# Kernel tuning notes

Measured on AMD Instinct MI355X. Metric: run time of the kernel, lower is better.

## Reference

```python
import jax, jax.numpy as jnp
import numpy as np

L, B, S, D, H, DH, V = 6, 2048, 64, 256, 8, 64, 100
INNER = H * DH          # 512
FF = 4 * D              # 1024 (GeGLU hidden after chunk)
SCALE = 8.0             # sqrt(DH)


def setup_inputs() -> dict:
    key = jax.random.key(0)
    ks = jax.random.split(key, 8)
    s = 0.02
    return {
        "x": jax.random.randint(ks[0], (B, S), 0, V),
        "E": jax.random.normal(ks[1], (S, V, D), dtype=jnp.float32) * s,
        "ln1_g": jnp.ones((L, D), jnp.float32),
        "ln1_b": jnp.zeros((L, D), jnp.float32),
        "Wqkv": jax.random.normal(ks[2], (L, D, 3 * INNER), dtype=jnp.float32) * s,
        "Wout": jax.random.normal(ks[3], (L, INNER, D), dtype=jnp.float32) * s,
        "bout": jnp.zeros((L, D), jnp.float32),
        "ln2_g": jnp.ones((L, D), jnp.float32),
        "ln2_b": jnp.zeros((L, D), jnp.float32),
        "W1": jax.random.normal(ks[4], (L, D, 2 * FF), dtype=jnp.float32) * s,
        "b1": jnp.zeros((L, 2 * FF), jnp.float32),
        "W2": jax.random.normal(ks[5], (L, FF, D), dtype=jnp.float32) * s,
        "b2": jnp.zeros((L, D), jnp.float32),
    }


def _ln(x, g, b):
    m = x.mean(-1, keepdims=True)
    v = ((x - m) ** 2).mean(-1, keepdims=True)
    return (x - m) * jax.lax.rsqrt(v + 1e-5) * g + b


def _split_heads(t):
    # [B,S,H*DH] -> [B,H,S,DH]
    return t.reshape(B, S, H, DH).transpose(0, 2, 1, 3)


def reference(x, E, ln1_g, ln1_b, Wqkv, Wout, bout, ln2_g, ln2_b, W1, b1, W2, b2):
    # per-column embedding lookup: E[col, x[b,col]] -> [B,S,D]
    h = E[jnp.arange(S)[None, :], x]
    for l in range(L):
        # PreNorm -> MHA
        n = _ln(h, ln1_g[l], ln1_b[l])
        qkv = n @ Wqkv[l]
        q, k, v = jnp.split(qkv, 3, axis=-1)
        q, k, v = _split_heads(q), _split_heads(k), _split_heads(v)
        score = jax.nn.softmax(
            jnp.einsum("bhqd,bhkd->bhqk", q, k) / SCALE, axis=-1
        )
        o = jnp.einsum("bhqk,bhkd->bhqd", score, v)
        o = o.transpose(0, 2, 1, 3).reshape(B, S, INNER)
        h = h + o @ Wout[l] + bout[l]
        # PreNorm -> GeGLU FFN
        n2 = _ln(h, ln2_g[l], ln2_b[l])
        u = n2 @ W1[l] + b1[l]
        a, g = jnp.split(u, 2, axis=-1)
        h = (a * jax.nn.gelu(g, approximate=False)) @ W2[l] + b2[l] + h
    return h
```

## Files before the change

### kernel.cpp

```cpp
#include <hip/hip_runtime.h>
#include <stdint.h>
#include <math.h>


#define LAYERS 6
#define BATCH  2048
#define SEQ    64
#define DMODEL 256
#define NHEAD  8
#define INNERD 512
#define FFDIM  1024
#define VOCAB  100
#define MTOK   (BATCH*SEQ)
#define MCAP   32768

typedef unsigned short u16;
typedef __attribute__((ext_vector_type(4))) float f32x4;
typedef __attribute__((ext_vector_type(4))) short s16x4;
typedef __attribute__((ext_vector_type(8))) short s16x8;

__device__ inline u16 f2bf(float f){
  union { float f; unsigned int u; } x; x.f = f;
  unsigned int u = x.u;
  return (u16)((u + 0x7fffu + ((u >> 16) & 1u)) >> 16);
}

__device__ inline void gload16(const void* g, void* l){
  __builtin_amdgcn_global_load_lds(
      (const __attribute__((address_space(1))) unsigned int*)g,
      (__attribute__((address_space(3))) unsigned int*)l, 16, 0, 0);
}

__device__ inline f32x4 mfma16(s16x8 a, s16x8 b, f32x4 c){
  return __builtin_amdgcn_mfma_f32_16x16x32_bf16(a, b, c, 0, 0, 0);
}

__device__ inline s16x8 ldfrag(const u16* lds, int row, int kk, int g){
  int chunk = ((kk<<2)|g) ^ (row&7);
  return *(const s16x8*)(lds + row*64 + chunk*8);
}

__device__ inline int pcol32(int col_base32, int hi, int g, int o){
  return col_base32 | (g<<3) | (hi<<2) | o;
}

__global__ __launch_bounds__(256) void wtrans_kernel(
    const float* __restrict__ in, u16* __restrict__ out, int K, int N, int total)
{
  int idx = blockIdx.x*256 + threadIdx.x;
  if (idx >= total) return;
  int l = idx / (N*K);
  int r = idx - l*(N*K);
  int n = r / K;
  int k = r - n*K;
  int p = (k & ~31) | (((k>>2)&3)<<3) | (((k>>4)&1)<<2) | (k&3);
  out[(size_t)l*N*K + (size_t)n*K + p] = f2bf(in[(size_t)l*K*N + (size_t)k*N + n]);
}

__global__ __launch_bounds__(256) void embed_ln_kernel(
    const int* __restrict__ x, const float* __restrict__ E,
    const float* __restrict__ gam, const float* __restrict__ bet,
    float* __restrict__ h, u16* __restrict__ nout)
{
  int t = threadIdx.x;
  int m = blockIdx.x*4 + (t>>6);
  int lane = t & 63;
  int s = m & 63;
  int tok = x[m];
  const float4 v = *(const float4*)(E + ((size_t)s*VOCAB + tok)*DMODEL + lane*4);
  *(float4*)(h + (size_t)m*DMODEL + lane*4) = v;
  float su = v.x+v.y+v.z+v.w;
  float q  = v.x*v.x+v.y*v.y+v.z*v.z+v.w*v.w;
  #pragma unroll
  for (int mask=1; mask<64; mask<<=1){
    su += __shfl_xor(su, mask);
    q  += __shfl_xor(q,  mask);
  }
  float mean = su*(1.f/256.f);
  float var  = q*(1.f/256.f) - mean*mean;
  float rs   = rsqrtf(var + 1e-5f);
  const float4 gv = *(const float4*)(gam + lane*4);
  const float4 bv = *(const float4*)(bet + lane*4);
  ushort4 ov;
  ov.x = f2bf((v.x-mean)*rs*gv.x + bv.x);
  ov.y = f2bf((v.y-mean)*rs*gv.y + bv.y);
  ov.z = f2bf((v.z-mean)*rs*gv.z + bv.z);
  ov.w = f2bf((v.w-mean)*rs*gv.w + bv.w);
  int p4 = (lane>>3)*32 + (lane&3)*8 + ((lane>>2)&1)*4;
  *(ushort4*)(nout + (size_t)m*DMODEL + p4) = ov;
}

__global__ __launch_bounds__(256, 3) void qkv_attn_kernel(
    const u16* __restrict__ A, const u16* __restrict__ Bt,
    u16* __restrict__ o, int K)
{
  __shared__ __align__(16) u16 smem[24576];
  u16* As = smem;
  u16* Bs = smem + 8192;
  u16* qs = smem;
  u16* ks = smem + 8192;
  u16* vt = smem + 16384;

  const int t = threadIdx.x;
  const int w = t >> 6, lane = t & 63, g = lane >> 4, c = lane & 15;
  const int cpx = gridDim.x >> 3;
  const int wg = (blockIdx.x & 7)*cpx + (blockIdx.x >> 3);
  const int hh = wg & 7;
  const int m0 = (wg >> 3) * 128;

  f32x4 acc[2][12];
  #pragma unroll
  for (int i=0;i<2;++i)
    #pragma unroll
    for (int j=0;j<12;++j){ f32x4 z = {0.f,0.f,0.f,0.f}; acc[i][j] = z; }

  const int nkt = K >> 6;
  for (int kt = 0; kt < nkt; ++kt){
    #pragma unroll
    for (int i=0;i<4;++i){
      int cid = (i*4 + w)*64 + lane;
      int row = cid >> 3, seg = cid & 7;
      gload16(A + (size_t)(m0+row)*K + (size_t)kt*64 + ((seg ^ (row&7))<<3),
              As + cid*8);
    }
    #pragma unroll
    for (int i=0;i<6;++i){
      int cid = (i*4 + w)*64 + lane;
      int brow = cid >> 3, seg = cid & 7;
      int ng = (brow>>6)*512 + hh*64 + (brow & 63);
      gload16(Bt + (size_t)ng*K + (size_t)kt*64 + ((seg ^ (brow&7))<<3),
              Bs + cid*8);
    }
    asm volatile("s_waitcnt vmcnt(0)" ::: "memory");
    __syncthreads();
    #pragma unroll
    for (int kk=0; kk<2; ++kk){
      s16x8 af[2];
      #pragma unroll
      for (int i=0;i<2;++i) af[i] = ldfrag(As, w*32 + i*16 + c, kk, g);
      #pragma unroll
      for (int j=0;j<12;++j){
        s16x8 bf = ldfrag(Bs, j*16 + c, kk, g);
        acc[0][j] = mfma16(af[0], bf, acc[0][j]);
        acc[1][j] = mfma16(af[1], bf, acc[1][j]);
      }
    }
    __syncthreads();
  }

  #pragma unroll
  for (int i=0;i<2;++i){
    #pragma unroll
    for (int j=0;j<12;++j){
      #pragma unroll
      for (int r=0;r<4;++r){
        int tl = w*32 + i*16 + g*4 + r;
        u16 val = f2bf(acc[i][j][r]);
        if (j < 8){
          int chunk = ((j&3)>>1)*4 + (c>>2);
          int pos   = (j&1)*4 + (c&3);
          u16* base = (j < 4) ? qs : ks;
          base[tl*64 + ((chunk ^ (tl&7))<<3) + pos] = val;
        } else {
          int d = (j-8)*16 + c;
          int row = (tl & 64) + d;
          int kcol = tl & 63;
          int chunk = ((kcol>>5)<<2) | ((kcol>>2)&3);
          int pos   = ((kcol>>4)&1)*4 + (kcol&3);
          vt[row*64 + ((chunk ^ (row&7))<<3) + pos] = val;
        }
      }
    }
  }
  __syncthreads();

  const int seq = w >> 1;
  const int qrow = w*32;

  f32x4 sc[4][2];
  #pragma unroll
  for (int jk=0;jk<4;++jk){ f32x4 z = {0.f,0.f,0.f,0.f}; sc[jk][0]=z; sc[jk][1]=z; }
  #pragma unroll
  for (int kk=0;kk<2;++kk){
    s16x8 qf0 = ldfrag(qs, qrow + c,      kk, g);
    s16x8 qf1 = ldfrag(qs, qrow + 16 + c, kk, g);
    #pragma unroll
    for (int jk=0;jk<4;++jk){
      s16x8 kf = ldfrag(ks, seq*64 + jk*16 + c, kk, g);
      sc[jk][0] = mfma16(kf, qf0, sc[jk][0]);
      sc[jk][1] = mfma16(kf, qf1, sc[jk][1]);
    }
  }

  s16x8 af[2][2];
  #pragma unroll
  for (int iq=0;iq<2;++iq){
    float mx = sc[0][iq][0];
    #pragma unroll
    for (int jk=0;jk<4;++jk)
      #pragma unroll
      for (int r=0;r<4;++r) mx = fmaxf(mx, sc[jk][iq][r]);
    mx = fmaxf(mx, __shfl_xor(mx, 16));
    mx = fmaxf(mx, __shfl_xor(mx, 32));
    float p[4][4];
    float sm = 0.f;
    #pragma unroll
    for (int jk=0;jk<4;++jk)
      #pragma unroll
      for (int r=0;r<4;++r){
        float e = expf((sc[jk][iq][r]-mx)*0.125f);
        p[jk][r] = e; sm += e;
      }
    sm += __shfl_xor(sm, 16);
    sm += __shfl_xor(sm, 32);
    float inv = 1.f/sm;
    #pragma unroll
    for (int kk=0;kk<2;++kk){
      union { s16x8 v; u16 e[8]; } u;
      #pragma unroll
      for (int oo=0;oo<4;++oo){
        u.e[oo]   = f2bf(p[2*kk  ][oo]*inv);
        u.e[4+oo] = f2bf(p[2*kk+1][oo]*inv);
      }
      af[iq][kk] = u.v;
    }
  }

  f32x4 oa[2][4];
  #pragma unroll
  for (int jd=0;jd<4;++jd){ f32x4 z = {0.f,0.f,0.f,0.f}; oa[0][jd]=z; oa[1][jd]=z; }
  #pragma unroll
  for (int kk=0;kk<2;++kk)
    #pragma unroll
    for (int jd=0;jd<4;++jd){
      s16x8 vf = ldfrag(vt, seq*64 + jd*16 + c, kk, g);
      oa[0][jd] = mfma16(af[0][kk], vf, oa[0][jd]);
      oa[1][jd] = mfma16(af[1][kk], vf, oa[1][jd]);
    }

  #pragma unroll
  for (int iq=0;iq<2;++iq){
    #pragma unroll
    for (int jd=0;jd<4;++jd){
      int col = hh*64 + jd*16 + c;
      int pc = pcol32(col & ~31, jd&1, c>>2, c&3);
      #pragma unroll
      for (int r=0;r<4;++r){
        int m = m0 + w*32 + iq*16 + g*4 + r;
        o[(size_t)m*INNERD + pc] = f2bf(oa[iq][jd][r]);
      }
    }
  }
}

__global__ __launch_bounds__(256, 2) void gemm_gated_kernel(
    const u16* __restrict__ A, const u16* __restrict__ Bt,
    u16* __restrict__ act, const float* __restrict__ b1, int K)
{
  __shared__ __align__(16) u16 As[128*64];
  __shared__ __align__(16) u16 Ba[128*64];
  __shared__ __align__(16) u16 Bg[128*64];
  const int t = threadIdx.x;
  const int w = t >> 6, lane = t & 63, g = lane >> 4, c = lane & 15;
  const int cpx = gridDim.x >> 3;
  const int wg = (blockIdx.x & 7)*cpx + (blockIdx.x >> 3);
  const int n0 = (wg & 7) * 128, m0 = (wg >> 3) * 128;
  const int wm = (w >> 1) * 64, wn = (w & 1) * 64;

  f32x4 acca[4][4], accg[4][4];
  #pragma unroll
  for (int i=0;i<4;++i)
    #pragma unroll
    for (int j=0;j<4;++j){ f32x4 z = {0.f,0.f,0.f,0.f}; acca[i][j] = z; accg[i][j] = z; }

  const int nkt = K >> 6;
  for (int kt = 0; kt < nkt; ++kt){
    #pragma unroll
    for (int i=0;i<4;++i){
      int cid = (i*4 + w)*64 + lane;
      int row = cid >> 3, qs = cid & 7;
      int col16 = ((qs ^ (row&7))<<3);
      gload16(A  + (size_t)(m0+row)*K      + (size_t)kt*64 + col16, As + (i*4+w)*512);
      gload16(Bt + (size_t)(n0+row)*K      + (size_t)kt*64 + col16, Ba + (i*4+w)*512);
      gload16(Bt + (size_t)(1024+n0+row)*K + (size_t)kt*64 + col16, Bg + (i*4+w)*512);
    }
    asm volatile("s_waitcnt vmcnt(0)" ::: "memory");
    __syncthreads();
    #pragma unroll
    for (int kk=0; kk<2; ++kk){
      s16x8 af[4];
      #pragma unroll
      for (int i=0;i<4;++i) af[i] = ldfrag(As, wm + i*16 + c, kk, g);
      #pragma unroll
      for (int j=0;j<4;++j){
        int row = wn + j*16 + c;
        s16x8 bfa = ldfrag(Ba, row, kk, g);
        s16x8 bfg = ldfrag(Bg, row, kk, g);
        #pragma unroll
        for (int i=0;i<4;++i){
          acca[i][j] = mfma16(af[i], bfa, acca[i][j]);
          accg[i][j] = mfma16(af[i], bfg, accg[i][j]);
        }
      }
    }
    __syncthreads();
  }

  #pragma unroll
  for (int i=0;i<4;++i)
    #pragma unroll
    for (int j=0;j<4;++j){
      int col = n0 + wn + j*16 + c;
      int pc = pcol32(col & ~31, j&1, c>>2, c&3);
      float ba = b1[col], bg = b1[1024 + col];
      #pragma unroll
      for (int r=0;r<4;++r){
        int m = m0 + wm + i*16 + g*4 + r;
        float ua = acca[i][j][r] + ba;
        float ug = accg[i][j][r] + bg;
        float gel = 0.5f*ug*(1.0f + erff(ug*0.70710678118654752f));
        act[(size_t)m*FFDIM + pc] = f2bf(ua*gel);
      }
    }
}

template<int DO_LN>
__global__ __launch_bounds__(256, 3) void gemm_res_ln_kernel(
    const u16* __restrict__ A, const u16* __restrict__ Bt,
    float* __restrict__ h, const float* __restrict__ bias,
    const float* __restrict__ gam, const float* __restrict__ bet,
    u16* __restrict__ nout, int K)
{
  __shared__ __align__(16) u16 As[64*64];
  __shared__ __align__(16) u16 Bs[256*64];
  __shared__ float ps[64][4];
  const int t = threadIdx.x;
  const int w = t >> 6, lane = t & 63, g = lane >> 4, c = lane & 15;
  const int wr = w >> 1, wc = w & 1;
  const int m0 = blockIdx.x * 64;

  f32x4 acc[2][8];
  #pragma unroll
  for (int i=0;i<2;++i)
    #pragma unroll
    for (int j=0;j<8;++j){ f32x4 z = {0.f,0.f,0.f,0.f}; acc[i][j] = z; }

  const int nkt = K >> 6;
  for (int kt = 0; kt < nkt; ++kt){
    #pragma unroll
    for (int i=0;i<2;++i){
      int cid = i*256 + t;
      int row = cid >> 3, qs = cid & 7;
      gload16(A + (size_t)(m0+row)*K + (size_t)kt*64 + ((qs ^ (row&7))<<3),
              As + cid*8);
    }
    #pragma unroll
    for (int i=0;i<8;++i){
      int cid = (i*4 + w)*64 + lane;
      int row = cid >> 3, qs = cid & 7;
      gload16(Bt + (size_t)row*K + (size_t)kt*64 + ((qs ^ (row&7))<<3),
              Bs + (i*4+w)*512);
    }
    asm volatile("s_waitcnt vmcnt(0)" ::: "memory");
    __syncthreads();
    #pragma unroll
    for (int kk=0; kk<2; ++kk){
      s16x8 af[2];
      #pragma unroll
      for (int i=0;i<2;++i) af[i] = ldfrag(As, wr*32 + i*16 + c, kk, g);
      #pragma unroll
      for (int j=0;j<8;++j){
        s16x8 bf = ldfrag(Bs, wc*128 + j*16 + c, kk, g);
        #pragma unroll
        for (int i=0;i<2;++i) acc[i][j] = mfma16(af[i], bf, acc[i][j]);
      }
    }
    __syncthreads();
  }

  #pragma unroll
  for (int i=0;i<2;++i){
    #pragma unroll
    for (int r=0;r<4;++r){
      int rl = wr*32 + i*16 + g*4 + r;
      size_t mrow = (size_t)(m0 + rl)*DMODEL;
      float s = 0.f, q2 = 0.f;
      #pragma unroll
      for (int j=0;j<8;++j){
        int col = wc*128 + j*16 + c;
        float v = acc[i][j][r] + bias[col] + h[mrow + col];
        h[mrow + col] = v;
        acc[i][j][r] = v;
        s += v; q2 += v*v;
      }
      if (DO_LN){
        #pragma unroll
        for (int mask=1; mask<16; mask<<=1){
          s  += __shfl_xor(s,  mask);
          q2 += __shfl_xor(q2, mask);
        }
        if (c == 0){ ps[rl][wc*2] = s; ps[rl][wc*2+1] = q2; }
      }
    }
  }
  if (DO_LN){
    __syncthreads();
    #pragma unroll
    for (int i=0;i<2;++i){
      #pragma unroll
      for (int r=0;r<4;++r){
        int rl = wr*32 + i*16 + g*4 + r;
        size_t mrow = (size_t)(m0 + rl)*DMODEL;
        float st = ps[rl][0] + ps[rl][2];
        float qt = ps[rl][1] + ps[rl][3];
        float mean = st*(1.f/256.f);
        float var  = qt*(1.f/256.f) - mean*mean;
        float rs   = rsqrtf(var + 1e-5f);
        #pragma unroll
        for (int j=0;j<8;++j){
          int col = wc*128 + j*16 + c;
          float v = acc[i][j][r];
          int pc = pcol32(col & ~31, j&1, c>>2, c&3);
          nout[mrow + pc] = f2bf((v-mean)*rs*gam[col] + bet[col]);
        }
      }
    }
  }
}

extern "C" void kernel_launch(void* const* d_in, const int* in_sizes, int n_in,
                              void* d_out, int out_size, void* d_ws, size_t ws_size,
                              hipStream_t stream)
{
  const int*   x    = (const int*)  d_in[0];
  const float* E    = (const float*)d_in[1];
  const float* ln1g = (const float*)d_in[2];
  const float* ln1b = (const float*)d_in[3];
  const float* Wqkv = (const float*)d_in[4];
  const float* Wout = (const float*)d_in[5];
  const float* bout = (const float*)d_in[6];
  const float* ln2g = (const float*)d_in[7];
  const float* ln2b = (const float*)d_in[8];
  const float* W1   = (const float*)d_in[9];
  const float* b1   = (const float*)d_in[10];
  const float* W2   = (const float*)d_in[11];
  const float* b2   = (const float*)d_in[12];
  float* h = (float*)d_out;

  const size_t WQKV = (size_t)LAYERS*1536*256;
  const size_t WOUT = (size_t)LAYERS*256*512;
  const size_t W1T  = (size_t)LAYERS*2048*256;
  const size_t W2T  = (size_t)LAYERS*256*1024;
  u16* wqkv_t = (u16*)d_ws;
  u16* wout_t = wqkv_t + WQKV;
  u16* w1_t   = wout_t + WOUT;
  u16* w2_t   = w1_t   + W1T;
  u16* abase  = w2_t   + W2T;
  const size_t wbytes = (WQKV + WOUT + W1T + W2T) * 2;
  if (ws_size < wbytes + (size_t)1024*3584) return;
  size_t rem = ws_size - wbytes;

  int Mc = MCAP;
  while (Mc > 1024 && (size_t)Mc*3584 > rem) Mc >>= 1;
  const int nc = MTOK / Mc;

  u16* n_bf   = abase;
  u16* o_bf   = n_bf + (size_t)Mc*256;
  u16* act_bf = o_bf + (size_t)Mc*512;

  int tot;
  tot = LAYERS*1536*256; wtrans_kernel<<<(tot+255)/256,256,0,stream>>>(Wqkv, wqkv_t, 256,  1536, tot);
  tot = LAYERS*256*512;  wtrans_kernel<<<(tot+255)/256,256,0,stream>>>(Wout, wout_t, 512,  256,  tot);
  tot = LAYERS*2048*256; wtrans_kernel<<<(tot+255)/256,256,0,stream>>>(W1,   w1_t,   256,  2048, tot);
  tot = LAYERS*256*1024; wtrans_kernel<<<(tot+255)/256,256,0,stream>>>(W2,   w2_t,   1024, 256,  tot);

  for (int cidx=0; cidx<nc; ++cidx){
    float* hc = h + (size_t)cidx*Mc*256;
    const int* xc = x + (size_t)cidx*Mc;
    embed_ln_kernel<<<Mc/4,256,0,stream>>>(xc, E, ln1g, ln1b, hc, n_bf);
    for (int l=0; l<LAYERS; ++l){
      qkv_attn_kernel<<<8*(Mc/128),256,0,stream>>>(
          n_bf, wqkv_t + (size_t)l*1536*256, o_bf, 256);
      gemm_res_ln_kernel<1><<<Mc/64,256,0,stream>>>(
          o_bf, wout_t + (size_t)l*256*512, hc, bout + l*256,
          ln2g + l*256, ln2b + l*256, n_bf, 512);
      gemm_gated_kernel<<<8*(Mc/128),256,0,stream>>>(
          n_bf, w1_t + (size_t)l*2048*256, act_bf, b1 + l*2048, 256);
      if (l < LAYERS-1){
        gemm_res_ln_kernel<1><<<Mc/64,256,0,stream>>>(
            act_bf, w2_t + (size_t)l*256*1024, hc, b2 + l*256,
            ln1g + (l+1)*256, ln1b + (l+1)*256, n_bf, 1024);
      } else {
        gemm_res_ln_kernel<0><<<Mc/64,256,0,stream>>>(
            act_bf, w2_t + (size_t)l*256*1024, hc, b2 + l*256,
            nullptr, nullptr, nullptr, 1024);
      }
    }
  }
}
```

Baseline: 3.899 ms.

## Double-buffer B tiles in gated GEMM and raise wave priority around MFMA loops

The gated FFN GEMM now hardcodes K=256 with a fully unrolled four-step K loop and double-buffers the two B tiles in LDS. The next B tiles are prefetched while the current step's MFMAs run, though the A tile is still loaded synchronously after each step. s_setprio hints are added around the MFMA sections in both the QKV/attention kernel and the gated kernel. LDS use in the gated kernel grows from 48KB to 80KB, which may reduce occupancy below the two blocks per CU requested by the launch bounds.

```diff
diff --git a/kernel.cpp b/kernel.cpp
--- a/kernel.cpp
+++ b/kernel.cpp
@@ -133,6 +133,7 @@
     }
     asm volatile("s_waitcnt vmcnt(0)" ::: "memory");
     __syncthreads();
+    __builtin_amdgcn_s_setprio(1);
     #pragma unroll
     for (int kk=0; kk<2; ++kk){
       s16x8 af[2];
@@ -145,6 +146,7 @@
         acc[1][j] = mfma16(af[1], bf, acc[1][j]);
       }
     }
+    __builtin_amdgcn_s_setprio(0);
     __syncthreads();
   }
 
@@ -180,6 +182,7 @@
   f32x4 sc[4][2];
   #pragma unroll
   for (int jk=0;jk<4;++jk){ f32x4 z = {0.f,0.f,0.f,0.f}; sc[jk][0]=z; sc[jk][1]=z; }
+  __builtin_amdgcn_s_setprio(1);
   #pragma unroll
   for (int kk=0;kk<2;++kk){
     s16x8 qf0 = ldfrag(qs, qrow + c,      kk, g);
@@ -191,6 +194,7 @@
       sc[jk][1] = mfma16(kf, qf1, sc[jk][1]);
     }
   }
+  __builtin_amdgcn_s_setprio(0);
 
   s16x8 af[2][2];
   #pragma unroll
@@ -229,6 +233,7 @@
   f32x4 oa[2][4];
   #pragma unroll
   for (int jd=0;jd<4;++jd){ f32x4 z = {0.f,0.f,0.f,0.f}; oa[0][jd]=z; oa[1][jd]=z; }
+  __builtin_amdgcn_s_setprio(1);
   #pragma unroll
   for (int kk=0;kk<2;++kk)
     #pragma unroll
@@ -237,6 +242,7 @@
       oa[0][jd] = mfma16(af[0][kk], vf, oa[0][jd]);
       oa[1][jd] = mfma16(af[1][kk], vf, oa[1][jd]);
     }
+  __builtin_amdgcn_s_setprio(0);
 
   #pragma unroll
   for (int iq=0;iq<2;++iq){
@@ -255,11 +261,10 @@
 
 __global__ __launch_bounds__(256, 2) void gemm_gated_kernel(
     const u16* __restrict__ A, const u16* __restrict__ Bt,
-    u16* __restrict__ act, const float* __restrict__ b1, int K)
+    u16* __restrict__ act, const float* __restrict__ b1)
 {
   __shared__ __align__(16) u16 As[128*64];
-  __shared__ __align__(16) u16 Ba[128*64];
-  __shared__ __align__(16) u16 Bg[128*64];
+  __shared__ __align__(16) u16 Bb[2][2][128*64];
   const int t = threadIdx.x;
   const int w = t >> 6, lane = t & 63, g = lane >> 4, c = lane & 15;
   const int cpx = gridDim.x >> 3;
@@ -273,19 +278,34 @@
     #pragma unroll
     for (int j=0;j<4;++j){ f32x4 z = {0.f,0.f,0.f,0.f}; acca[i][j] = z; accg[i][j] = z; }
 
-  const int nkt = K >> 6;
-  for (int kt = 0; kt < nkt; ++kt){
-    #pragma unroll
-    for (int i=0;i<4;++i){
-      int cid = (i*4 + w)*64 + lane;
-      int row = cid >> 3, qs = cid & 7;
-      int col16 = ((qs ^ (row&7))<<3);
-      gload16(A  + (size_t)(m0+row)*K      + (size_t)kt*64 + col16, As + (i*4+w)*512);
-      gload16(Bt + (size_t)(n0+row)*K      + (size_t)kt*64 + col16, Ba + (i*4+w)*512);
-      gload16(Bt + (size_t)(1024+n0+row)*K + (size_t)kt*64 + col16, Bg + (i*4+w)*512);
-    }
-    asm volatile("s_waitcnt vmcnt(0)" ::: "memory");
-    __syncthreads();
+  #pragma unroll
+  for (int i=0;i<4;++i){
+    int cid = (i*4 + w)*64 + lane;
+    int row = cid >> 3, seg = cid & 7;
+    int col16 = ((seg ^ (row&7))<<3);
+    gload16(A  + (size_t)(m0+row)*256      + col16, As + cid*8);
+    gload16(Bt + (size_t)(n0+row)*256      + col16, Bb[0][0] + cid*8);
+    gload16(Bt + (size_t)(1024+n0+row)*256 + col16, Bb[0][1] + cid*8);
+  }
+  asm volatile("s_waitcnt vmcnt(0)" ::: "memory");
+  __syncthreads();
+
+  #pragma unroll
+  for (int kt = 0; kt < 4; ++kt){
+    const int cur = kt & 1;
+    if (kt < 3){
+      #pragma unroll
+      for (int i=0;i<4;++i){
+        int cid = (i*4 + w)*64 + lane;
+        int row = cid >> 3, seg = cid & 7;
+        int col16 = ((seg ^ (row&7))<<3);
+        gload16(Bt + (size_t)(n0+row)*256      + (size_t)(kt+1)*64 + col16,
+                Bb[cur^1][0] + cid*8);
+        gload16(Bt + (size_t)(1024+n0+row)*256 + (size_t)(kt+1)*64 + col16,
+                Bb[cur^1][1] + cid*8);
+      }
+    }
+    __builtin_amdgcn_s_setprio(1);
     #pragma unroll
     for (int kk=0; kk<2; ++kk){
       s16x8 af[4];
@@ -294,8 +314,8 @@
       #pragma unroll
       for (int j=0;j<4;++j){
         int row = wn + j*16 + c;
-        s16x8 bfa = ldfrag(Ba, row, kk, g);
-        s16x8 bfg = ldfrag(Bg, row, kk, g);
+        s16x8 bfa = ldfrag(Bb[cur][0], row, kk, g);
+        s16x8 bfg = ldfrag(Bb[cur][1], row, kk, g);
         #pragma unroll
         for (int i=0;i<4;++i){
           acca[i][j] = mfma16(af[i], bfa, acca[i][j]);
@@ -303,7 +323,19 @@
         }
       }
     }
+    __builtin_amdgcn_s_setprio(0);
     __syncthreads();
+    if (kt < 3){
+      #pragma unroll
+      for (int i=0;i<4;++i){
+        int cid = (i*4 + w)*64 + lane;
+        int row = cid >> 3, seg = cid & 7;
+        gload16(A + (size_t)(m0+row)*256 + (size_t)(kt+1)*64 + ((seg ^ (row&7))<<3),
+                As + cid*8);
+      }
+      asm volatile("s_waitcnt vmcnt(0)" ::: "memory");
+      __syncthreads();
+    }
   }
 
   #pragma unroll
@@ -485,7 +517,7 @@
           o_bf, wout_t + (size_t)l*256*512, hc, bout + l*256,
           ln2g + l*256, ln2b + l*256, n_bf, 512);
       gemm_gated_kernel<<<8*(Mc/128),256,0,stream>>>(
-          n_bf, w1_t + (size_t)l*2048*256, act_bf, b1 + l*2048, 256);
+          n_bf, w1_t + (size_t)l*2048*256, act_bf, b1 + l*2048);
       if (l < LAYERS-1){
         gemm_res_ln_kernel<1><<<Mc/64,256,0,stream>>>(
             act_bf, w2_t + (size_t)l*256*1024, hc, b2 + l*256,
```

Result: no change. 3.923 ms (+0.6%).
